# Kernel optimization log

Measured on AMD Instinct MI355X. Metric: run time of the kernel, lower is better.

The kernel has to match this reference:

```python
import jax, jax.numpy as jnp
import numpy as np

B, N, D = 8, 1024, 1024

def setup_inputs() -> dict:
    key = jax.random.key(0)
    k1, k2, k3, k4, k5 = jax.random.split(key, 5)
    x = jax.random.normal(k1, (B, N, D), dtype=jnp.float32)
    y = jax.random.normal(k2, (B, N, D), dtype=jnp.float32)
    adj = jax.random.uniform(k3, (B, N, N), dtype=jnp.float32)
    adj_sumrow = jnp.sum(adj, axis=-1, keepdims=True)  # [B, N, 1], row-sum normalizer
    W = jax.random.normal(k4, (D, D), dtype=jnp.float32) * (1.0 / np.sqrt(D))
    b = jax.random.normal(k5, (D,), dtype=jnp.float32) * 0.02
    return {"x": x, "y": y, "adj": adj, "adj_sumrow": adj_sumrow, "W": W, "b": b}

def reference(x, y, adj, adj_sumrow, W, b):
    # GraphConvolutionCustom: project neighbor features, aggregate via dense adj,
    # normalize by row-sum, add bias and residual input x; then ReLU.
    # Dropout is identity in eval mode (training=False).
    support = jnp.einsum('bnd,de->bne', y, W)          # [B, N, D]
    agg = jnp.matmul(adj, support) / adj_sumrow        # [B, N, D]
    out = jax.nn.relu(agg + b + x)
    return out
```

## Files before the change

kernel.cpp:

```cpp
#include <hip/hip_runtime.h>
#include <hip/hip_bf16.h>
#include <stdint.h>


typedef float  f32x4  __attribute__((ext_vector_type(4)));
typedef __bf16 bf16x8 __attribute__((ext_vector_type(8)));

__device__ __forceinline__ unsigned short f2bf(float f) {
  union { float f; unsigned int u; } c; c.f = f;
  unsigned int u = c.u;
  u += 0x7FFFu + ((u >> 16) & 1u);
  return (unsigned short)(u >> 16);
}

__device__ __forceinline__ void async_cp16(const void* g, void* l) {
  __builtin_amdgcn_global_load_lds(
      (const __attribute__((address_space(1))) unsigned int*)g,
      (__attribute__((address_space(3))) unsigned int*)l, 16, 0, 0);
}


__global__ void k_cvt(const float4* __restrict__ src, ushort4* __restrict__ dst, int n4) {
  int i = blockIdx.x * blockDim.x + threadIdx.x;
  if (i >= n4) return;
  float4 v = src[i];
  ushort4 p;
  p.x = f2bf(v.x); p.y = f2bf(v.y); p.z = f2bf(v.z); p.w = f2bf(v.w);
  dst[i] = p;
}

__global__ void k_transpose_cvt(const float* __restrict__ W, unsigned short* __restrict__ Wt) {
  __shared__ float t[64][65];
  const int tx = threadIdx.x, ty = threadIdx.y;
  const int n0 = blockIdx.x * 64, k0 = blockIdx.y * 64;
#pragma unroll
  for (int r = ty; r < 64; r += 4)
    t[r][tx] = W[(size_t)(k0 + r) * 1024 + n0 + tx];
  __syncthreads();
#pragma unroll
  for (int r = ty; r < 64; r += 4)
    Wt[(size_t)(n0 + r) * 1024 + k0 + tx] = f2bf(t[tx][r]);
}


__device__ __forceinline__ void gemm_mainloop(
    const unsigned short* __restrict__ A,
    const unsigned short* __restrict__ Bt,
    int m0, int n0, f32x4 acc[4][4],
    unsigned short* lA, unsigned short* lB, int tid)
{
  const int lane = tid & 63;
  const int wave = tid >> 6;
  const int wm   = (wave >> 1) * 64;
  const int wn   = (wave & 1) * 64;
  const int quad = lane >> 4;
  const int l16  = lane & 15;
  const int srow = lane >> 2;
  const int scol = (lane & 3) * 8;

#pragma unroll 1
  for (int k0 = 0; k0 < 1024; k0 += 32) {
#pragma unroll
    for (int s = 0; s < 2; ++s) {
      const int c = wave * 2 + s;
      async_cp16(A  + (((size_t)(m0 + c * 16 + srow)) << 10) + k0 + scol, lA + c * 512);
      async_cp16(Bt + (((size_t)(n0 + c * 16 + srow)) << 10) + k0 + scol, lB + c * 512);
    }
    __syncthreads();

    bf16x8 af[4], bfr[4];
#pragma unroll
    for (int i = 0; i < 4; ++i)
      af[i]  = *(const bf16x8*)(lA + (wm + i * 16 + l16) * 32 + quad * 8);
#pragma unroll
    for (int j = 0; j < 4; ++j)
      bfr[j] = *(const bf16x8*)(lB + (wn + j * 16 + l16) * 32 + quad * 8);

#pragma unroll
    for (int i = 0; i < 4; ++i)
#pragma unroll
      for (int j = 0; j < 4; ++j)
        acc[i][j] = __builtin_amdgcn_mfma_f32_16x16x32_bf16(af[i], bfr[j], acc[i][j], 0, 0, 0);
    __syncthreads();
  }
}


__global__ __launch_bounds__(256) void k_gemm1(
    const unsigned short* __restrict__ Ybf,
    const unsigned short* __restrict__ Wt,
    unsigned short* __restrict__ SupT)
{
  __shared__ __align__(16) unsigned short lA[128 * 32];
  __shared__ __align__(16) unsigned short lB[128 * 32];
  const int tid = threadIdx.x;
  const int n0 = blockIdx.x * 128, m0 = blockIdx.y * 128, b = blockIdx.z;

  f32x4 acc[4][4];
#pragma unroll
  for (int i = 0; i < 4; ++i)
#pragma unroll
    for (int j = 0; j < 4; ++j)
#pragma unroll
      for (int r = 0; r < 4; ++r) acc[i][j][r] = 0.0f;

  gemm_mainloop(Ybf + ((size_t)b << 20), Wt, m0, n0, acc, lA, lB, tid);

  unsigned short* Sb = SupT + ((size_t)b << 20);
  const int lane = tid & 63, wave = tid >> 6;
  const int wm = (wave >> 1) * 64, wn = (wave & 1) * 64;
  const int quad = lane >> 4, l16 = lane & 15;
#pragma unroll
  for (int i = 0; i < 4; ++i) {
    const int mb = m0 + wm + i * 16 + quad * 4;
#pragma unroll
    for (int j = 0; j < 4; ++j) {
      const int n = n0 + wn + j * 16 + l16;
      ushort4 p;
      p.x = f2bf(acc[i][j][0]); p.y = f2bf(acc[i][j][1]);
      p.z = f2bf(acc[i][j][2]); p.w = f2bf(acc[i][j][3]);
      *(ushort4*)(Sb + (((size_t)n) << 10) + mb) = p;
    }
  }
}


__global__ __launch_bounds__(256) void k_gemm2(
    const unsigned short* __restrict__ AdjBf,
    const unsigned short* __restrict__ SupT,
    const float* __restrict__ x,
    const float* __restrict__ sumrow,
    const float* __restrict__ bias,
    float* __restrict__ out)
{
  __shared__ __align__(16) unsigned short lA[128 * 32];
  __shared__ __align__(16) unsigned short lB[128 * 32];
  const int tid = threadIdx.x;
  const int n0 = blockIdx.x * 128, m0 = blockIdx.y * 128, b = blockIdx.z;

  f32x4 acc[4][4];
#pragma unroll
  for (int i = 0; i < 4; ++i)
#pragma unroll
    for (int j = 0; j < 4; ++j)
#pragma unroll
      for (int r = 0; r < 4; ++r) acc[i][j][r] = 0.0f;

  gemm_mainloop(AdjBf + ((size_t)b << 20), SupT + ((size_t)b << 20), m0, n0, acc, lA, lB, tid);

  const float* xb = x   + ((size_t)b << 20);
  float*       ob = out + ((size_t)b << 20);
  const float* sr = sumrow + ((size_t)b << 10);
  const int lane = tid & 63, wave = tid >> 6;
  const int wm = (wave >> 1) * 64, wn = (wave & 1) * 64;
  const int quad = lane >> 4, l16 = lane & 15;

  float bv[4];
#pragma unroll
  for (int j = 0; j < 4; ++j) bv[j] = bias[n0 + wn + j * 16 + l16];

#pragma unroll
  for (int i = 0; i < 4; ++i) {
    const int mb = m0 + wm + i * 16 + quad * 4;
#pragma unroll
    for (int r = 0; r < 4; ++r) {
      const int m = mb + r;
      const float inv = 1.0f / sr[m];
#pragma unroll
      for (int j = 0; j < 4; ++j) {
        const int n = n0 + wn + j * 16 + l16;
        const size_t idx = (((size_t)m) << 10) + n;
        float v = acc[i][j][r] * inv + bv[j] + xb[idx];
        ob[idx] = fmaxf(v, 0.0f);
      }
    }
  }
}


extern "C" void kernel_launch(void* const* d_in, const int* in_sizes, int n_in,
                              void* d_out, int out_size, void* d_ws, size_t ws_size,
                              hipStream_t stream) {
  const float* x      = (const float*)d_in[0];
  const float* y      = (const float*)d_in[1];
  const float* adj    = (const float*)d_in[2];
  const float* sumrow = (const float*)d_in[3];
  const float* W      = (const float*)d_in[4];
  const float* bias   = (const float*)d_in[5];
  float* out = (float*)d_out;

  char* ws = (char*)d_ws;
  unsigned short* ybf   = (unsigned short*)(ws);
  unsigned short* adjbf = (unsigned short*)(ws + ((size_t)16 << 20));
  unsigned short* wt    = (unsigned short*)(ws + ((size_t)32 << 20));
  unsigned short* supT  = (unsigned short*)(ws + ((size_t)34 << 20));

  const int n4 = (8 << 20) / 4;
  k_cvt<<<dim3(n4 / 256), dim3(256), 0, stream>>>((const float4*)y,   (ushort4*)ybf,   n4);
  k_cvt<<<dim3(n4 / 256), dim3(256), 0, stream>>>((const float4*)adj, (ushort4*)adjbf, n4);
  k_transpose_cvt<<<dim3(16, 16), dim3(64, 4), 0, stream>>>(W, wt);
  k_gemm1<<<dim3(8, 8, 8), dim3(256), 0, stream>>>(ybf, wt, supT);
  k_gemm2<<<dim3(8, 8, 8), dim3(256), 0, stream>>>(adjbf, supT, x, sumrow, bias, out);
}
```

Baseline: 225.6 us.

## Use K=64 swizzled LDS tiles and batch-fused transposed first GEMM

Doubles the K step of the shared GEMM main loop to 64 and adds an XOR-style column swizzle in LDS to avoid bank conflicts, halving the number of barriers per tile. The first GEMM is recast as Wt × Y^T over all batches at once (N=8192), writing support in a [D, B*N] layout that the second GEMM reads with stride 8192. This removes the per-batch reload of W and the strided transposed store, at the cost of doubled LDS usage per block and scalar 2-byte stores in the first GEMM epilogue.

```diff
diff --git a/kernel.cpp b/kernel.cpp
--- a/kernel.cpp
+++ b/kernel.cpp
@@ -43,9 +43,9 @@
 }
 
 
-__device__ __forceinline__ void gemm_mainloop(
-    const unsigned short* __restrict__ A,
-    const unsigned short* __restrict__ Bt,
+__device__ __forceinline__ void gemm_mainloop64(
+    const unsigned short* __restrict__ A,  int strideA,
+    const unsigned short* __restrict__ Bt, int strideB,
     int m0, int n0, f32x4 acc[4][4],
     unsigned short* lA, unsigned short* lB, int tid)
 {
@@ -55,58 +55,66 @@
   const int wn   = (wave & 1) * 64;
   const int quad = lane >> 4;
   const int l16  = lane & 15;
-  const int srow = lane >> 2;
-  const int scol = (lane & 3) * 8;
+  const int rg   = lane >> 3;
+  const int colo = (((lane & 7) - rg) & 7) * 8;
 
 #pragma unroll 1
-  for (int k0 = 0; k0 < 1024; k0 += 32) {
-#pragma unroll
-    for (int s = 0; s < 2; ++s) {
-      const int c = wave * 2 + s;
-      async_cp16(A  + (((size_t)(m0 + c * 16 + srow)) << 10) + k0 + scol, lA + c * 512);
-      async_cp16(Bt + (((size_t)(n0 + c * 16 + srow)) << 10) + k0 + scol, lB + c * 512);
+  for (int k0 = 0; k0 < 1024; k0 += 64) {
+#pragma unroll
+    for (int s = 0; s < 4; ++s) {
+      const int t = wave * 4 + s;
+      async_cp16(A  + (size_t)(m0 + t * 8 + rg) * strideA + k0 + colo, lA + t * 512);
+      async_cp16(Bt + (size_t)(n0 + t * 8 + rg) * strideB + k0 + colo, lB + t * 512);
     }
     __syncthreads();
 
-    bf16x8 af[4], bfr[4];
-#pragma unroll
-    for (int i = 0; i < 4; ++i)
-      af[i]  = *(const bf16x8*)(lA + (wm + i * 16 + l16) * 32 + quad * 8);
-#pragma unroll
-    for (int j = 0; j < 4; ++j)
-      bfr[j] = *(const bf16x8*)(lB + (wn + j * 16 + l16) * 32 + quad * 8);
-
-#pragma unroll
-    for (int i = 0; i < 4; ++i)
-#pragma unroll
-      for (int j = 0; j < 4; ++j)
-        acc[i][j] = __builtin_amdgcn_mfma_f32_16x16x32_bf16(af[i], bfr[j], acc[i][j], 0, 0, 0);
+#pragma unroll
+    for (int h = 0; h < 2; ++h) {
+      bf16x8 af[4], bfr[4];
+#pragma unroll
+      for (int i = 0; i < 4; ++i) {
+        const int r = wm + i * 16 + l16;
+        af[i]  = *(const bf16x8*)(lA + r * 64 + ((h * 4 + quad + r) & 7) * 8);
+      }
+#pragma unroll
+      for (int j = 0; j < 4; ++j) {
+        const int r = wn + j * 16 + l16;
+        bfr[j] = *(const bf16x8*)(lB + r * 64 + ((h * 4 + quad + r) & 7) * 8);
+      }
+#pragma unroll
+      for (int i = 0; i < 4; ++i)
+#pragma unroll
+        for (int j = 0; j < 4; ++j)
+          acc[i][j] = __builtin_amdgcn_mfma_f32_16x16x32_bf16(af[i], bfr[j], acc[i][j], 0, 0, 0);
+    }
     __syncthreads();
   }
 }
 
+__device__ __forceinline__ void zero_acc(f32x4 acc[4][4]) {
+#pragma unroll
+  for (int i = 0; i < 4; ++i)
+#pragma unroll
+    for (int j = 0; j < 4; ++j)
+#pragma unroll
+      for (int r = 0; r < 4; ++r) acc[i][j][r] = 0.0f;
+}
+
 
 __global__ __launch_bounds__(256) void k_gemm1(
+    const unsigned short* __restrict__ Wt,
     const unsigned short* __restrict__ Ybf,
-    const unsigned short* __restrict__ Wt,
-    unsigned short* __restrict__ SupT)
+    unsigned short* __restrict__ Sup2)
 {
-  __shared__ __align__(16) unsigned short lA[128 * 32];
-  __shared__ __align__(16) unsigned short lB[128 * 32];
+  __shared__ __align__(16) unsigned short lA[128 * 64];
+  __shared__ __align__(16) unsigned short lB[128 * 64];
   const int tid = threadIdx.x;
-  const int n0 = blockIdx.x * 128, m0 = blockIdx.y * 128, b = blockIdx.z;
+  const int n0 = blockIdx.x * 128, m0 = blockIdx.y * 128;
 
   f32x4 acc[4][4];
-#pragma unroll
-  for (int i = 0; i < 4; ++i)
-#pragma unroll
-    for (int j = 0; j < 4; ++j)
-#pragma unroll
-      for (int r = 0; r < 4; ++r) acc[i][j][r] = 0.0f;
-
-  gemm_mainloop(Ybf + ((size_t)b << 20), Wt, m0, n0, acc, lA, lB, tid);
-
-  unsigned short* Sb = SupT + ((size_t)b << 20);
+  zero_acc(acc);
+  gemm_mainloop64(Wt, 1024, Ybf, 1024, m0, n0, acc, lA, lB, tid);
+
   const int lane = tid & 63, wave = tid >> 6;
   const int wm = (wave >> 1) * 64, wn = (wave & 1) * 64;
   const int quad = lane >> 4, l16 = lane & 15;
@@ -114,12 +122,11 @@
   for (int i = 0; i < 4; ++i) {
     const int mb = m0 + wm + i * 16 + quad * 4;
 #pragma unroll
-    for (int j = 0; j < 4; ++j) {
-      const int n = n0 + wn + j * 16 + l16;
-      ushort4 p;
-      p.x = f2bf(acc[i][j][0]); p.y = f2bf(acc[i][j][1]);
-      p.z = f2bf(acc[i][j][2]); p.w = f2bf(acc[i][j][3]);
-      *(ushort4*)(Sb + (((size_t)n) << 10) + mb) = p;
+    for (int r = 0; r < 4; ++r) {
+      unsigned short* row = Sup2 + ((size_t)(mb + r) << 13);
+#pragma unroll
+      for (int j = 0; j < 4; ++j)
+        row[n0 + wn + j * 16 + l16] = f2bf(acc[i][j][r]);
     }
   }
 }
@@ -127,26 +134,22 @@
 
 __global__ __launch_bounds__(256) void k_gemm2(
     const unsigned short* __restrict__ AdjBf,
-    const unsigned short* __restrict__ SupT,
+    const unsigned short* __restrict__ Sup2,
     const float* __restrict__ x,
     const float* __restrict__ sumrow,
     const float* __restrict__ bias,
     float* __restrict__ out)
 {
-  __shared__ __align__(16) unsigned short lA[128 * 32];
-  __shared__ __align__(16) unsigned short lB[128 * 32];
+  __shared__ __align__(16) unsigned short lA[128 * 64];
+  __shared__ __align__(16) unsigned short lB[128 * 64];
   const int tid = threadIdx.x;
   const int n0 = blockIdx.x * 128, m0 = blockIdx.y * 128, b = blockIdx.z;
 
   f32x4 acc[4][4];
-#pragma unroll
-  for (int i = 0; i < 4; ++i)
-#pragma unroll
-    for (int j = 0; j < 4; ++j)
-#pragma unroll
-      for (int r = 0; r < 4; ++r) acc[i][j][r] = 0.0f;
-
-  gemm_mainloop(AdjBf + ((size_t)b << 20), SupT + ((size_t)b << 20), m0, n0, acc, lA, lB, tid);
+  zero_acc(acc);
+  gemm_mainloop64(AdjBf + ((size_t)b << 20), 1024,
+                  Sup2 + ((size_t)b << 10), 8192,
+                  m0, n0, acc, lA, lB, tid);
 
   const float* xb = x   + ((size_t)b << 20);
   float*       ob = out + ((size_t)b << 20);
@@ -193,12 +196,12 @@
   unsigned short* ybf   = (unsigned short*)(ws);
   unsigned short* adjbf = (unsigned short*)(ws + ((size_t)16 << 20));
   unsigned short* wt    = (unsigned short*)(ws + ((size_t)32 << 20));
-  unsigned short* supT  = (unsigned short*)(ws + ((size_t)34 << 20));
+  unsigned short* sup2  = (unsigned short*)(ws + ((size_t)34 << 20));
 
   const int n4 = (8 << 20) / 4;
   k_cvt<<<dim3(n4 / 256), dim3(256), 0, stream>>>((const float4*)y,   (ushort4*)ybf,   n4);
   k_cvt<<<dim3(n4 / 256), dim3(256), 0, stream>>>((const float4*)adj, (ushort4*)adjbf, n4);
   k_transpose_cvt<<<dim3(16, 16), dim3(64, 4), 0, stream>>>(W, wt);
-  k_gemm1<<<dim3(8, 8, 8), dim3(256), 0, stream>>>(ybf, wt, supT);
-  k_gemm2<<<dim3(8, 8, 8), dim3(256), 0, stream>>>(adjbf, supT, x, sumrow, bias, out);
-}
+  k_gemm1<<<dim3(64, 8), dim3(256), 0, stream>>>(wt, ybf, sup2);
+  k_gemm2<<<dim3(8, 8, 8), dim3(256), 0, stream>>>(adjbf, sup2, x, sumrow, bias, out);
+}
```

Result: faster. 207.1 us (-8.2%).
